# Performance work log

Measured on AMD Instinct MI355X. Metric: run time of the kernel, lower is better.

Reference implementation:

```python
import jax, jax.numpy as jnp
import numpy as np

B, C, T = 32, 64, 2500
SFREQ = 250
KW_S = 0.5
K = int(KW_S * SFREQ)          # 125-tap wavelet kernel
F = 10                          # n_freqs_init
OCT_MIN, OCT_MAX = 0.0, 3.0
N_OUT = 2
HID = 8
VEC = C * (C + 1) // 2          # 2080 upper-tri vectorization dim
FEAT = F * VEC                  # 20800
EPS = 1e-5


def setup_inputs() -> dict:
    key = jax.random.key(0)
    ks = jax.random.split(key, 4)
    X = jax.random.normal(ks[0], (B, C, T), jnp.float32)
    # wavelet params (octave-scaled), as in Green.__init__ with random_f_init=False
    foi = jnp.linspace(OCT_MIN, OCT_MAX, F).astype(jnp.float32)
    fwhm = -jnp.linspace(OCT_MIN - 1.0, OCT_MAX - 1.0, F).astype(jnp.float32)
    shrink = jnp.float32(-3.0)                       # pre-sigmoid shrinkage
    brn_w = jnp.ones((VEC,), jnp.float32)            # BatchReNorm scale (rebias=False)
    bn1_g = jnp.ones((FEAT,), jnp.float32)
    bn1_b = jnp.zeros((FEAT,), jnp.float32)
    W1 = jax.random.normal(ks[1], (HID, FEAT), jnp.float32) / np.sqrt(FEAT)
    b1 = jnp.zeros((HID,), jnp.float32)
    bn2_g = jnp.ones((HID,), jnp.float32)
    bn2_b = jnp.zeros((HID,), jnp.float32)
    W2 = jax.random.normal(ks[2], (N_OUT, HID), jnp.float32) / np.sqrt(HID)
    b2 = jnp.zeros((N_OUT,), jnp.float32)
    return dict(X=X, foi=foi, fwhm=fwhm, shrink=shrink, brn_w=brn_w,
                bn1_g=bn1_g, bn1_b=bn1_b, W1=W1, b1=b1,
                bn2_g=bn2_g, bn2_b=bn2_b, W2=W2, b2=b2)


def reference(X, foi, fwhm, shrink, brn_w, bn1_g, bn1_b, W1, b1, bn2_g, bn2_b, W2, b2):
    # ---- WaveletConv: Gabor (Morlet) bank, octave scaling, VALID conv, stride 1 ----
    t = (jnp.arange(K, dtype=jnp.float32) - (K - 1) / 2.0) / SFREQ   # (K,) seconds
    f_hz = 2.0 ** foi                                                # (F,)
    fwhm_s = 2.0 ** fwhm                                             # (F,) seconds
    sigma = fwhm_s / (2.0 * jnp.sqrt(2.0 * jnp.log(2.0)))
    env = jnp.exp(-0.5 * (t[None, :] / sigma[:, None]) ** 2)         # (F,K)
    env = env / jnp.sum(env, axis=1, keepdims=True)                  # unit-mass envelope
    phase = 2.0 * jnp.pi * f_hz[:, None] * t[None, :]
    kern = jnp.concatenate([env * jnp.cos(phase), env * jnp.sin(phase)], 0)[:, None, :]  # (2F,1,K)
    Xr = X.reshape(B * C, 1, T)
    Y = jax.lax.conv_general_dilated(Xr, kern, (1,), 'VALID',
                                     dimension_numbers=('NCH', 'OIH', 'NCH'))  # (B*C,2F,Tc)
    Tc = Y.shape[-1]                                 # T - K + 1 = 2376
    Y = Y.reshape(B, C, 2 * F, Tc)
    Zr, Zi = Y[:, :, :F], Y[:, :, F:]                # real/imag parts, (B,C,F,Tc)
    # ---- real covariance pooling: Re(Z Z^H)/Tc per (batch, freq) ----
    Ccov = (jnp.einsum('bcft,bdft->bfcd', Zr, Zr)
            + jnp.einsum('bcft,bdft->bfcd', Zi, Zi)) / Tc            # (B,F,C,C)
    # ---- learnable shrinkage toward scaled identity ----
    alpha = jax.nn.sigmoid(shrink)
    mu = jnp.mean(jnp.diagonal(Ccov, axis1=-2, axis2=-1), axis=-1)   # (B,F)
    Cs = (1.0 - alpha) * Ccov + alpha * mu[..., None, None] * jnp.eye(C, dtype=Ccov.dtype)
    # ---- LogEig: batched matrix log + upper-tri vectorization (sqrt2 off-diag) ----
    w, V = jnp.linalg.eigh(Cs)
    logC = jnp.einsum('bfij,bfj,bfkj->bfik', V, jnp.log(w), V)       # (B,F,C,C)
    iu, ju = jnp.triu_indices(C)
    scale = jnp.where(iu == ju, 1.0, jnp.sqrt(2.0)).astype(logC.dtype)
    vec = logC[..., iu, ju] * scale                                  # (B,F,VEC)
    # ---- BatchReNorm (scale only, stats over batch and freq axes) ----
    m = jnp.mean(vec, (0, 1))
    v = jnp.var(vec, (0, 1))
    vec = (vec - m) / jnp.sqrt(v + EPS) * brn_w
    # ---- head: BN -> Linear -> GELU(exact) -> BN -> Linear (dropout = eval/identity) ----
    h = vec.reshape(B, FEAT)
    h = (h - h.mean(0)) / jnp.sqrt(h.var(0) + EPS) * bn1_g + bn1_b
    h = h @ W1.T + b1
    h = jax.nn.gelu(h, approximate=False)
    h = (h - h.mean(0)) / jnp.sqrt(h.var(0) + EPS) * bn2_g + bn2_b
    return h @ W2.T + b2
```

## Files before the change

### kernel.cpp

```cpp
#include <hip/hip_runtime.h>
#include <math.h>

#define NSWEEP 12

#define WS_T16 0
#define WS_IU  2048
#define WS_JU  4128
#define WS_MU  6208
#define WS_SC  8288
#define WS_ACC 10368
#define WS_COV 16384
#define WS_VEC (16384 + 320*4096)
#define WS_Z   1994752

typedef _Float16 f16x8 __attribute__((ext_vector_type(8)));
typedef float f32x16 __attribute__((ext_vector_type(16)));

union H8 { int4 i; f16x8 h; };
union HP { uint32_t u; _Float16 h[2]; };

__device__ inline f32x16 zero16() {
    f32x16 z;
#pragma unroll
    for (int r = 0; r < 16; r++) z[r] = 0.0f;
    return z;
}

__global__ void k0_build(const float* __restrict__ foi, const float* __restrict__ fwhm,
                         _Float16* __restrict__ T16,
                         int* __restrict__ iu, int* __restrict__ ju) {
    __shared__ float env[128];
    __shared__ float ssum;
    int tid = threadIdx.x;
    for (int u = tid; u < 2080; u += 256) {
        int i = 0, off = 0;
        while (off + (64 - i) <= u) { off += (64 - i); i++; }
        iu[u] = i;
        ju[u] = i + (u - off);
    }
    for (int idx = tid; idx < 32 * 128; idx += 256) T16[idx] = (_Float16)0.0f;
    __syncthreads();
    const float inv_sfreq = 1.0f / 250.0f;
    for (int f = 0; f < 10; f++) {
        float fhz = exp2f(foi[f]);
        float sig = exp2f(fwhm[f]) / (2.0f * sqrtf(2.0f * logf(2.0f)));
        if (tid < 128) {
            float e = 0.0f;
            if (tid < 125) {
                float t = ((float)tid - 62.0f) * inv_sfreq;
                float z = t / sig;
                e = expf(-0.5f * z * z);
            }
            env[tid] = e;
        }
        __syncthreads();
        if (tid == 0) {
            float s = 0.0f;
            for (int k = 0; k < 125; k++) s += env[k];
            ssum = s;
        }
        __syncthreads();
        if (tid < 125) {
            float e = env[tid] / ssum;
            float t = ((float)tid - 62.0f) * inv_sfreq;
            float ph = 6.283185307179586f * fhz * t;
            T16[f * 128 + tid] = (_Float16)(e * cosf(ph));
            T16[(10 + f) * 128 + tid] = (_Float16)(e * sinf(ph));
        }
        __syncthreads();
    }
}

__global__ __launch_bounds__(256) void kconv(const float* __restrict__ X,
                                             const _Float16* __restrict__ T16,
                                             _Float16* __restrict__ Zbuf,
                                             int t0chunk, int Tpad, int subs) {
    __shared__ __align__(16) uint32_t P[64 * 256];
    int tid = threadIdx.x;
    int b = blockIdx.x / subs;
    int sub = blockIdx.x - b * subs;
    int tbase = t0chunk + sub * 128;
    const float* Xb = X + b * (64 * 2500);
    bool fastblk = (tbase + 256 < 2500);
    for (int task = tid; task < 64 * 64; task += 256) {
        int c = task >> 6, grp = task & 63;
        int t = tbase + grp * 4;
        const float* src = Xb + c * 2500 + t;
        float x0, x1, x2, x3, x4;
        if (fastblk) {
            float4 v = *(const float4*)src;
            x0 = v.x; x1 = v.y; x2 = v.z; x3 = v.w; x4 = src[4];
        } else {
            x0 = (t + 0 < 2500) ? src[0] : 0.0f;
            x1 = (t + 1 < 2500) ? src[1] : 0.0f;
            x2 = (t + 2 < 2500) ? src[2] : 0.0f;
            x3 = (t + 3 < 2500) ? src[3] : 0.0f;
            x4 = (t + 4 < 2500) ? src[4] : 0.0f;
        }
        HP p0, p1, p2, p3;
        p0.h[0] = (_Float16)x0; p0.h[1] = (_Float16)x1;
        p1.h[0] = (_Float16)x1; p1.h[1] = (_Float16)x2;
        p2.h[0] = (_Float16)x2; p2.h[1] = (_Float16)x3;
        p3.h[0] = (_Float16)x3; p3.h[1] = (_Float16)x4;
        uint4 up; up.x = p0.u; up.y = p1.u; up.z = p2.u; up.w = p3.u;
        *(uint4*)&P[c * 256 + grp * 4] = up;
    }
    __syncthreads();
    int lane = tid & 63;
    int w = tid >> 6;
    int n = lane & 31, g = lane >> 5;
    H8 a[8];
#pragma unroll
    for (int ks = 0; ks < 8; ks++)
        a[ks].i = *(const int4*)(T16 + n * 128 + ks * 16 + g * 8);
    int tw = w * 32;
    int colg = tbase + tw + n;
    bool colok = (colg < 2376);
    int tloc = sub * 128 + tw + n;
    int zb0 = b * 1280;
    for (int c = 0; c < 64; c++) {
        f32x16 acc = zero16();
        const uint32_t* Pc = &P[c * 256 + tw + n + 8 * g];
#pragma unroll
        for (int ks = 0; ks < 8; ks++) {
            H8 bv;
            bv.i.x = (int)Pc[16 * ks + 0];
            bv.i.y = (int)Pc[16 * ks + 2];
            bv.i.z = (int)Pc[16 * ks + 4];
            bv.i.w = (int)Pc[16 * ks + 6];
            acc = __builtin_amdgcn_mfma_f32_32x32x16_f16(a[ks].h, bv.h, acc, 0, 0, 0);
        }
        if (colok) {
            int zb = zb0 + c;
#pragma unroll
            for (int r = 0; r < 16; r++) {
                int row = (r & 3) + 8 * (r >> 2) + 4 * g;
                if (row < 20)
                    Zbuf[(zb + row * 64) * Tpad + tloc] = (_Float16)acc[r];
            }
        }
    }
}

__global__ __launch_bounds__(256) void kcov(const _Float16* __restrict__ Zbuf,
                                            float* __restrict__ cov,
                                            int t0chunk, int Tcur, int Tpad) {
    __shared__ __align__(16) _Float16 Zs[2][64 * 100];
    int tid = threadIdx.x;
    int lane = tid & 63, w = tid >> 6;
    int n = lane & 31, g = lane >> 5;
    int bf = blockIdx.x;
    int b = bf / 10, f = bf - b * 10;
    const _Float16* Zr = Zbuf + (size_t)((b * 20 + f) * 64) * Tpad;
    const _Float16* Zi = Zbuf + (size_t)((b * 20 + 10 + f) * 64) * Tpad;
    int ti = w >> 1, tj = w & 1;
    f32x16 acc = zero16();
    int limit = min(Tcur, 2376 - t0chunk);
    int nsub = (limit + 95) / 96;
    for (int sc = 0; sc < nsub; sc++) {
        int tl0 = sc * 96;
        __syncthreads();
        for (int task = tid; task < 1536; task += 256) {
            int arr = task / 768;
            int rem = task - arr * 768;
            int c = rem / 12;
            int o = (rem - c * 12) * 8;
            int tg = tl0 + o;
            const _Float16* src = (arr ? Zi : Zr) + c * Tpad + tg;
            H8 v;
            if (tg + 8 <= limit) {
                v.i = *(const int4*)src;
            } else {
#pragma unroll
                for (int j2 = 0; j2 < 8; j2++)
                    v.h[j2] = (tg + j2 < limit) ? src[j2] : (_Float16)0.0f;
            }
            *(int2*)&Zs[arr][c * 100 + o] = make_int2(v.i.x, v.i.y);
            *(int2*)&Zs[arr][c * 100 + o + 4] = make_int2(v.i.z, v.i.w);
        }
        __syncthreads();
        int ra = (32 * ti + n) * 100 + g * 8;
        int rb = (32 * tj + n) * 100 + g * 8;
#pragma unroll
        for (int arr = 0; arr < 2; arr++) {
#pragma unroll
            for (int ks = 0; ks < 6; ks++) {
                const _Float16* pa = &Zs[arr][ra + ks * 16];
                const _Float16* pb = &Zs[arr][rb + ks * 16];
                int2 a0 = *(const int2*)pa;
                int2 a1 = *(const int2*)(pa + 4);
                int2 b0 = *(const int2*)pb;
                int2 b1 = *(const int2*)(pb + 4);
                H8 av, bv;
                av.i = make_int4(a0.x, a0.y, a1.x, a1.y);
                bv.i = make_int4(b0.x, b0.y, b1.x, b1.y);
                acc = __builtin_amdgcn_mfma_f32_32x32x16_f16(av.h, bv.h, acc, 0, 0, 0);
            }
        }
    }
    float* covbf = cov + bf * 4096;
    int col = 32 * tj + n;
#pragma unroll
    for (int r = 0; r < 16; r++) {
        int row = 32 * ti + (r & 3) + 8 * (r >> 2) + 4 * g;
        covbf[row * 64 + col] += acc[r];
    }
}

__global__ __launch_bounds__(64) void keja(float* __restrict__ cov,
                                           const float* __restrict__ shrink,
                                           float* __restrict__ dvec,
                                           float* __restrict__ dmu) {
    int s = threadIdx.x;
    int bf = blockIdx.x;
    float* C = cov + bf * 4096;
    float w[64];
#pragma unroll
    for (int r = 0; r < 64; r++) w[r] = C[r * 64 + s];
    float ts = C[s * 65];
#pragma unroll
    for (int m = 1; m < 64; m <<= 1) ts += __shfl_xor(ts, m, 64);
    float mu = ts * (1.0f / (64.0f * 2376.0f));
    float alpha = 1.0f / (1.0f + expf(-shrink[0]));
    float scl = (1.0f - alpha) / (2376.0f * fmaxf(mu, 1e-30f));
#pragma unroll
    for (int r = 0; r < 64; r++) {
        float v = w[r] * scl;
        if (r == s) v += alpha;
        w[r] = v;
    }
    for (int sweep = 0; sweep < NSWEEP; sweep++) {
        float n0 = 0, n1 = 0, n2 = 0, n3 = 0;
#pragma unroll
        for (int r = 0; r < 64; r += 4) {
            n0 = fmaf(w[r], w[r], n0);
            n1 = fmaf(w[r + 1], w[r + 1], n1);
            n2 = fmaf(w[r + 2], w[r + 2], n2);
            n3 = fmaf(w[r + 3], w[r + 3], n3);
        }
        float nrm = (n0 + n1) + (n2 + n3);
        for (int m = 1; m < 64; m++) {
            int addr = (s ^ m) << 2;
            float q[64];
#pragma unroll
            for (int r = 0; r < 64; r++)
                q[r] = __int_as_float(__builtin_amdgcn_ds_bpermute(addr, __float_as_int(w[r])));
            float d0 = 0, d1 = 0, d2 = 0, d3 = 0;
#pragma unroll
            for (int r = 0; r < 64; r += 4) {
                d0 = fmaf(w[r], q[r], d0);
                d1 = fmaf(w[r + 1], q[r + 1], d1);
                d2 = fmaf(w[r + 2], q[r + 2], d2);
                d3 = fmaf(w[r + 3], q[r + 3], d3);
            }
            float dpq = (d0 + d1) + (d2 + d3);
            float pn = __int_as_float(__builtin_amdgcn_ds_bpermute(addr, __float_as_int(nrm)));
            int h = 31 - __builtin_clz((unsigned)m);
            bool top = (((s >> h) & 1) == 0);
            float dpp = top ? nrm : pn;
            float dqq = top ? pn : nrm;
            bool rot = (dpq * dpq > 1e-13f * dpp * dqq);
            float tau = (dqq - dpp) / (2.0f * dpq);
            float tt = 1.0f / (fabsf(tau) + sqrtf(1.0f + tau * tau));
            if (tau < 0.0f) tt = -tt;
            if (!rot) tt = 0.0f;
            float cc = rsqrtf(1.0f + tt * tt);
            float ssn = tt * cc;
            float sg = top ? -ssn : ssn;
#pragma unroll
            for (int r = 0; r < 64; r++)
                w[r] = cc * w[r] + sg * q[r];
            nrm = fmaf(top ? -tt : tt, dpq, nrm);
        }
    }
    float n0 = 0, n1 = 0, n2 = 0, n3 = 0;
#pragma unroll
    for (int r = 0; r < 64; r += 4) {
        n0 = fmaf(w[r], w[r], n0);
        n1 = fmaf(w[r + 1], w[r + 1], n1);
        n2 = fmaf(w[r + 2], w[r + 2], n2);
        n3 = fmaf(w[r + 3], w[r + 3], n3);
    }
    float nrm = (n0 + n1) + (n2 + n3);
    float d = 0.5f * logf(nrm) / nrm;
#pragma unroll
    for (int r = 0; r < 64; r++) C[r * 64 + s] = w[r];
    dvec[bf * 64 + s] = d;
    if (s == 0) dmu[bf] = logf(fmaxf(mu, 1e-30f));
}

__global__ __launch_bounds__(256) void kvec(const float* __restrict__ W,
                                            const float* __restrict__ dvec,
                                            const float* __restrict__ dmu,
                                            const int* __restrict__ iu,
                                            const int* __restrict__ ju,
                                            float* __restrict__ vec) {
    __shared__ float WL[64 * 68];
    __shared__ float WD[64 * 68];
    __shared__ float ds[64];
    int tid = threadIdx.x;
    int bf = blockIdx.x;
    const float* Wb = W + bf * 4096;
    if (tid < 64) ds[tid] = dvec[bf * 64 + tid];
    __syncthreads();
    for (int idx = tid; idx < 4096; idx += 256) {
        int i = idx >> 6, c = idx & 63;
        float v = Wb[idx];
        WL[i * 68 + c] = v;
        WD[i * 68 + c] = v * ds[c];
    }
    __syncthreads();
    float logmu = dmu[bf];
    float* out = vec + bf * 2080;
    for (int u = tid; u < 2080; u += 256) {
        int i = iu[u], j = ju[u];
        const float* a = &WD[i * 68];
        const float* b = &WL[j * 68];
        float s0 = 0, s1 = 0, s2 = 0, s3 = 0;
#pragma unroll
        for (int k = 0; k < 64; k += 16) {
            float4 a0 = *(const float4*)(a + k);
            float4 b0 = *(const float4*)(b + k);
            float4 a1 = *(const float4*)(a + k + 4);
            float4 b1 = *(const float4*)(b + k + 4);
            float4 a2 = *(const float4*)(a + k + 8);
            float4 b2 = *(const float4*)(b + k + 8);
            float4 a3 = *(const float4*)(a + k + 12);
            float4 b3 = *(const float4*)(b + k + 12);
            s0 = fmaf(a0.x, b0.x, fmaf(a0.y, b0.y, fmaf(a0.z, b0.z, fmaf(a0.w, b0.w, s0))));
            s1 = fmaf(a1.x, b1.x, fmaf(a1.y, b1.y, fmaf(a1.z, b1.z, fmaf(a1.w, b1.w, s1))));
            s2 = fmaf(a2.x, b2.x, fmaf(a2.y, b2.y, fmaf(a2.z, b2.z, fmaf(a2.w, b2.w, s2))));
            s3 = fmaf(a3.x, b3.x, fmaf(a3.y, b3.y, fmaf(a3.z, b3.z, fmaf(a3.w, b3.w, s3))));
        }
        float ssm = (s0 + s1) + (s2 + s3);
        if (i == j) ssm += logmu;
        else ssm *= 1.4142135623730951f;
        out[u] = ssm;
    }
}

__global__ void k3a_stats(const float* __restrict__ vec, const float* __restrict__ brn_w,
                          float* __restrict__ m_u, float* __restrict__ sc_u) {
    int u = blockIdx.x * 256 + threadIdx.x;
    if (u >= 2080) return;
    float s1 = 0.0f, s2 = 0.0f;
    for (int bfi = 0; bfi < 320; bfi++) {
        float x = vec[bfi * 2080 + u];
        s1 += x; s2 += x * x;
    }
    float m = s1 * (1.0f / 320.0f);
    float v = s2 * (1.0f / 320.0f) - m * m;
    m_u[u] = m;
    sc_u[u] = brn_w[u] * rsqrtf(v + 1e-5f);
}

__global__ __launch_bounds__(256) void k3b_bn1mm(const float* __restrict__ vec,
                                                 const float* __restrict__ m_u,
                                                 const float* __restrict__ sc_u,
                                                 const float* __restrict__ g1,
                                                 const float* __restrict__ bb1,
                                                 const float* __restrict__ W1,
                                                 float* __restrict__ acc) {
    __shared__ float hbuf[256 * 33];
    __shared__ float wbuf[8 * 256];
    int tid = threadIdx.x;
    int j = blockIdx.x * 256 + tid;
    bool act = (j < 20800);
    int f = act ? (j / 2080) : 0;
    int u = act ? (j % 2080) : 0;
    float mm = act ? m_u[u] : 0.0f;
    float sc = act ? sc_u[u] : 0.0f;
    float xv[32];
    float s1 = 0.0f, s2 = 0.0f;
    for (int b = 0; b < 32; b++) {
        float x = act ? ((vec[(b * 10 + f) * 2080 + u] - mm) * sc) : 0.0f;
        xv[b] = x;
        s1 += x; s2 += x * x;
    }
    float m1 = s1 * (1.0f / 32.0f);
    float inv1 = rsqrtf(s2 * (1.0f / 32.0f) - m1 * m1 + 1e-5f);
    float gg = act ? g1[j] : 0.0f;
    float bb = act ? bb1[j] : 0.0f;
    for (int b = 0; b < 32; b++)
        hbuf[tid * 33 + b] = (xv[b] - m1) * inv1 * gg + bb;
    for (int hid = 0; hid < 8; hid++)
        wbuf[hid * 256 + tid] = act ? W1[hid * 20800 + j] : 0.0f;
    __syncthreads();
    int b = tid >> 3, hid = tid & 7;
    float ssm = 0.0f;
    for (int jj = 0; jj < 256; jj++)
        ssm += hbuf[jj * 33 + b] * wbuf[hid * 256 + jj];
    atomicAdd(&acc[b * 8 + hid], ssm);
}

__global__ void k4_final(const float* __restrict__ acc, const float* __restrict__ b1,
                         const float* __restrict__ bn2g, const float* __restrict__ bn2b,
                         const float* __restrict__ W2, const float* __restrict__ b2,
                         float* __restrict__ out) {
    __shared__ float gl[256];
    __shared__ float m2[8], i2[8];
    int tid = threadIdx.x;
    int b = tid >> 3, hid = tid & 7;
    float x = acc[tid] + b1[hid];
    float ge = 0.5f * x * (1.0f + erff(x * 0.7071067811865476f));
    gl[tid] = ge;
    __syncthreads();
    if (tid < 8) {
        float s1 = 0.0f, s2 = 0.0f;
        for (int bb = 0; bb < 32; bb++) {
            float v = gl[bb * 8 + tid];
            s1 += v; s2 += v * v;
        }
        float mm = s1 * (1.0f / 32.0f);
        m2[tid] = mm;
        i2[tid] = rsqrtf(s2 * (1.0f / 32.0f) - mm * mm + 1e-5f);
    }
    __syncthreads();
    float h2 = (ge - m2[hid]) * i2[hid] * bn2g[hid] + bn2b[hid];
    gl[tid] = h2;
    __syncthreads();
    if (tid < 64) {
        int bo = tid >> 1, o = tid & 1;
        float ssm = b2[o];
        for (int hh = 0; hh < 8; hh++) ssm += gl[bo * 8 + hh] * W2[o * 8 + hh];
        out[bo * 2 + o] = ssm;
    }
}

extern "C" void kernel_launch(void* const* d_in, const int* in_sizes, int n_in,
                              void* d_out, int out_size, void* d_ws, size_t ws_size,
                              hipStream_t stream) {
    const float* X     = (const float*)d_in[0];
    const float* foi   = (const float*)d_in[1];
    const float* fwhm  = (const float*)d_in[2];
    const float* shrink= (const float*)d_in[3];
    const float* brn_w = (const float*)d_in[4];
    const float* bn1_g = (const float*)d_in[5];
    const float* bn1_b = (const float*)d_in[6];
    const float* W1    = (const float*)d_in[7];
    const float* b1    = (const float*)d_in[8];
    const float* bn2_g = (const float*)d_in[9];
    const float* bn2_b = (const float*)d_in[10];
    const float* W2    = (const float*)d_in[11];
    const float* b2    = (const float*)d_in[12];

    float* ws    = (float*)d_ws;
    _Float16* T16= (_Float16*)(ws + WS_T16);
    int*   iu    = (int*)(ws + WS_IU);
    int*   ju    = (int*)(ws + WS_JU);
    float* m_u   = ws + WS_MU;
    float* sc_u  = ws + WS_SC;
    float* acc   = ws + WS_ACC;
    float* cov   = ws + WS_COV;
    float* vec   = ws + WS_VEC;
    _Float16* Zbuf = (_Float16*)(ws + WS_Z);
    float* dvec  = (float*)(ws + WS_Z);
    float* dmuv  = dvec + 320 * 64;

    size_t zavail = (ws_size > (size_t)WS_Z * 4) ? ws_size - (size_t)WS_Z * 4 : 0;
    const int cand[6] = {2432, 1152, 768, 384, 256, 128};
    int Tchunk = 128;
    for (int i = 0; i < 6; i++) {
        if (81920ull * (size_t)cand[i] <= zavail) { Tchunk = cand[i]; break; }
    }

    hipMemsetAsync(cov, 0, 320 * 4096 * sizeof(float), stream);
    hipMemsetAsync(acc, 0, 256 * sizeof(float), stream);

    k0_build<<<1, 256, 0, stream>>>(foi, fwhm, T16, iu, ju);
    for (int t0 = 0; t0 < 2376; t0 += Tchunk) {
        int Tcur = min(Tchunk, 2376 - t0);
        int subs = (Tcur + 127) / 128;
        kconv<<<32 * subs, 256, 0, stream>>>(X, T16, Zbuf, t0, Tchunk, subs);
        kcov<<<320, 256, 0, stream>>>(Zbuf, cov, t0, Tcur, Tchunk);
    }
    keja<<<320, 64, 0, stream>>>(cov, shrink, dvec, dmuv);
    kvec<<<320, 256, 0, stream>>>(cov, dvec, dmuv, iu, ju, vec);
    k3a_stats<<<9, 256, 0, stream>>>(vec, brn_w, m_u, sc_u);
    k3b_bn1mm<<<82, 256, 0, stream>>>(vec, m_u, sc_u, bn1_g, bn1_b, W1, acc);
    k4_final<<<1, 256, 0, stream>>>(acc, b1, bn2_g, bn2_b, W2, b2, (float*)d_out);
}
```

Baseline: 845.6 us.

## Cut Jacobi sweeps, chunk bpermute exchanges, use fast rcp/sqrt intrinsics

The one-sided Jacobi eigen kernel drops from 12 to 9 sweeps. The 64-register partner column is now fetched in double-buffered 8-element chunks of ds_bpermute, re-fetched for the rotation update instead of held, which cuts register pressure. The rotation-angle maths uses hardware rcp/sqrt/rsq intrinsics. Fewer sweeps risk less converged eigendecompositions, and the extra bpermute pass adds LDS traffic.

```diff
diff --git a/kernel.cpp b/kernel.cpp
--- a/kernel.cpp
+++ b/kernel.cpp
@@ -1,7 +1,7 @@
 #include <hip/hip_runtime.h>
 #include <math.h>
 
-#define NSWEEP 12
+#define NSWEEP 9
 
 #define WS_T16 0
 #define WS_IU  2048
@@ -24,6 +24,10 @@
 #pragma unroll
     for (int r = 0; r < 16; r++) z[r] = 0.0f;
     return z;
+}
+
+__device__ __forceinline__ float bperm(int addr, float v) {
+    return __int_as_float(__builtin_amdgcn_ds_bpermute(addr, __float_as_int(v)));
 }
 
 __global__ void k0_build(const float* __restrict__ foi, const float* __restrict__ fwhm,
@@ -207,10 +211,10 @@
     }
 }
 
-__global__ __launch_bounds__(64) void keja(float* __restrict__ cov,
-                                           const float* __restrict__ shrink,
-                                           float* __restrict__ dvec,
-                                           float* __restrict__ dmu) {
+__global__ __launch_bounds__(64, 1) void keja5(float* __restrict__ cov,
+                                               const float* __restrict__ shrink,
+                                               float* __restrict__ dvec,
+                                               float* __restrict__ dmu) {
     int s = threadIdx.x;
     int bf = blockIdx.x;
     float* C = cov + bf * 4096;
@@ -229,47 +233,73 @@
         if (r == s) v += alpha;
         w[r] = v;
     }
+    float nrm = 0.0f;
     for (int sweep = 0; sweep < NSWEEP; sweep++) {
-        float n0 = 0, n1 = 0, n2 = 0, n3 = 0;
-#pragma unroll
-        for (int r = 0; r < 64; r += 4) {
-            n0 = fmaf(w[r], w[r], n0);
-            n1 = fmaf(w[r + 1], w[r + 1], n1);
-            n2 = fmaf(w[r + 2], w[r + 2], n2);
-            n3 = fmaf(w[r + 3], w[r + 3], n3);
-        }
-        float nrm = (n0 + n1) + (n2 + n3);
+        {
+            float n0 = 0, n1 = 0, n2 = 0, n3 = 0;
+#pragma unroll
+            for (int r = 0; r < 64; r += 4) {
+                n0 = fmaf(w[r], w[r], n0);
+                n1 = fmaf(w[r + 1], w[r + 1], n1);
+                n2 = fmaf(w[r + 2], w[r + 2], n2);
+                n3 = fmaf(w[r + 3], w[r + 3], n3);
+            }
+            nrm = (n0 + n1) + (n2 + n3);
+        }
         for (int m = 1; m < 64; m++) {
             int addr = (s ^ m) << 2;
-            float q[64];
-#pragma unroll
-            for (int r = 0; r < 64; r++)
-                q[r] = __int_as_float(__builtin_amdgcn_ds_bpermute(addr, __float_as_int(w[r])));
+            float pn = bperm(addr, nrm);
+            float q[2][8];
+#pragma unroll
+            for (int r = 0; r < 8; r++) q[0][r] = bperm(addr, w[r]);
             float d0 = 0, d1 = 0, d2 = 0, d3 = 0;
 #pragma unroll
-            for (int r = 0; r < 64; r += 4) {
-                d0 = fmaf(w[r], q[r], d0);
-                d1 = fmaf(w[r + 1], q[r + 1], d1);
-                d2 = fmaf(w[r + 2], q[r + 2], d2);
-                d3 = fmaf(w[r + 3], q[r + 3], d3);
+            for (int c = 0; c < 8; c++) {
+                if (c < 7) {
+#pragma unroll
+                    for (int r = 0; r < 8; r++)
+                        q[(c + 1) & 1][r] = bperm(addr, w[(c + 1) * 8 + r]);
+                }
+                const float* qc = q[c & 1];
+                int base = c * 8;
+                d0 = fmaf(w[base + 0], qc[0], d0);
+                d1 = fmaf(w[base + 1], qc[1], d1);
+                d2 = fmaf(w[base + 2], qc[2], d2);
+                d3 = fmaf(w[base + 3], qc[3], d3);
+                d0 = fmaf(w[base + 4], qc[4], d0);
+                d1 = fmaf(w[base + 5], qc[5], d1);
+                d2 = fmaf(w[base + 6], qc[6], d2);
+                d3 = fmaf(w[base + 7], qc[7], d3);
             }
             float dpq = (d0 + d1) + (d2 + d3);
-            float pn = __int_as_float(__builtin_amdgcn_ds_bpermute(addr, __float_as_int(nrm)));
             int h = 31 - __builtin_clz((unsigned)m);
             bool top = (((s >> h) & 1) == 0);
             float dpp = top ? nrm : pn;
             float dqq = top ? pn : nrm;
             bool rot = (dpq * dpq > 1e-13f * dpp * dqq);
-            float tau = (dqq - dpp) / (2.0f * dpq);
-            float tt = 1.0f / (fabsf(tau) + sqrtf(1.0f + tau * tau));
-            if (tau < 0.0f) tt = -tt;
+            float tau = (dqq - dpp) * 0.5f * __builtin_amdgcn_rcpf(dpq);
+            float tt = __builtin_amdgcn_rcpf(fabsf(tau) +
+                        __builtin_amdgcn_sqrtf(fmaf(tau, tau, 1.0f)));
+            tt = (tau < 0.0f) ? -tt : tt;
             if (!rot) tt = 0.0f;
-            float cc = rsqrtf(1.0f + tt * tt);
+            float cc = __builtin_amdgcn_rsqf(fmaf(tt, tt, 1.0f));
             float ssn = tt * cc;
             float sg = top ? -ssn : ssn;
 #pragma unroll
-            for (int r = 0; r < 64; r++)
-                w[r] = cc * w[r] + sg * q[r];
+            for (int r = 0; r < 8; r++) q[0][r] = bperm(addr, w[r]);
+#pragma unroll
+            for (int c = 0; c < 8; c++) {
+                if (c < 7) {
+#pragma unroll
+                    for (int r = 0; r < 8; r++)
+                        q[(c + 1) & 1][r] = bperm(addr, w[(c + 1) * 8 + r]);
+                }
+                const float* qc = q[c & 1];
+                int base = c * 8;
+#pragma unroll
+                for (int r = 0; r < 8; r++)
+                    w[base + r] = fmaf(cc, w[base + r], sg * qc[r]);
+            }
             nrm = fmaf(top ? -tt : tt, dpq, nrm);
         }
     }
@@ -281,11 +311,10 @@
         n2 = fmaf(w[r + 2], w[r + 2], n2);
         n3 = fmaf(w[r + 3], w[r + 3], n3);
     }
-    float nrm = (n0 + n1) + (n2 + n3);
-    float d = 0.5f * logf(nrm) / nrm;
+    float nf = (n0 + n1) + (n2 + n3);
 #pragma unroll
     for (int r = 0; r < 64; r++) C[r * 64 + s] = w[r];
-    dvec[bf * 64 + s] = d;
+    dvec[bf * 64 + s] = 0.5f * logf(nf) / nf;
     if (s == 0) dmu[bf] = logf(fmaxf(mu, 1e-30f));
 }
 
@@ -474,7 +503,7 @@
         kconv<<<32 * subs, 256, 0, stream>>>(X, T16, Zbuf, t0, Tchunk, subs);
         kcov<<<320, 256, 0, stream>>>(Zbuf, cov, t0, Tcur, Tchunk);
     }
-    keja<<<320, 64, 0, stream>>>(cov, shrink, dvec, dmuv);
+    keja5<<<320, 64, 0, stream>>>(cov, shrink, dvec, dmuv);
     kvec<<<320, 256, 0, stream>>>(cov, dvec, dmuv, iu, ju, vec);
     k3a_stats<<<9, 256, 0, stream>>>(vec, brn_w, m_u, sc_u);
     k3b_bn1mm<<<82, 256, 0, stream>>>(vec, m_u, sc_u, bn1_g, bn1_b, W1, acc);
```

Measured after the change: 680.2 us. 1.24x faster.
